# Kernel optimization log

Hardware: AMD Instinct MI355X
Metric: run time of the kernel (lower is better)

Reference implementation:

```python
import jax, jax.numpy as jnp
import numpy as np

B, L, T_ENC = 32, 64, 196
INPUT, EMBED, HIDDEN, VOCAB = 2048, 512, 512, 32000
SCALE = 1.0 / float(512 ** 0.5)


def setup_inputs() -> dict:
    key = jax.random.key(0)
    ks = jax.random.split(key, 24)
    s = 0.05
    embed_table = jax.random.normal(ks[3], (VOCAB, EMBED)) * s
    embed_table = embed_table.at[0].set(0.0)  # padding_idx=0
    d = {
        "features": jax.random.normal(ks[0], (B, INPUT)),
        "captions": jax.random.randint(ks[1], (B, L), 0, VOCAB, dtype=jnp.int32),
        "lengths": jnp.full((B,), L, dtype=jnp.int32),
        "encoder_outputs": jax.random.normal(ks[2], (B, T_ENC, 512)),
        "embed_table": embed_table,
        "ft1_w": jax.random.normal(ks[4], (HIDDEN, INPUT)) * s,
        "ft1_b": jax.random.normal(ks[5], (HIDDEN,)) * s,
        "ft2_w": jax.random.normal(ks[6], (HIDDEN, HIDDEN)) * s,
        "ft2_b": jax.random.normal(ks[7], (HIDDEN,)) * s,
        # torch LSTM gate order: i, f, g, o; layer0 input = embed+512
        "w_ih0": jax.random.normal(ks[8], (4 * HIDDEN, EMBED + 512)) * s,
        "w_hh0": jax.random.normal(ks[9], (4 * HIDDEN, HIDDEN)) * s,
        "b_ih0": jax.random.normal(ks[10], (4 * HIDDEN,)) * s,
        "b_hh0": jax.random.normal(ks[11], (4 * HIDDEN,)) * s,
        "w_ih1": jax.random.normal(ks[12], (4 * HIDDEN, HIDDEN)) * s,
        "w_hh1": jax.random.normal(ks[13], (4 * HIDDEN, HIDDEN)) * s,
        "b_ih1": jax.random.normal(ks[14], (4 * HIDDEN,)) * s,
        "b_hh1": jax.random.normal(ks[15], (4 * HIDDEN,)) * s,
        "fc_w": jax.random.normal(ks[16], (VOCAB, HIDDEN)) * s,
        "fc_b": jax.random.normal(ks[17], (VOCAB,)) * s,
    }
    return d


def _lstm_cell(x, h, c, w_ih, w_hh, b_ih, b_hh):
    g = x @ w_ih.T + h @ w_hh.T + b_ih + b_hh
    i, f, gg, o = jnp.split(g, 4, axis=-1)
    c2 = jax.nn.sigmoid(f) * c + jax.nn.sigmoid(i) * jnp.tanh(gg)
    h2 = jax.nn.sigmoid(o) * jnp.tanh(c2)
    return h2, c2


def reference(features, captions, lengths, encoder_outputs, embed_table,
              ft1_w, ft1_b, ft2_w, ft2_b,
              w_ih0, w_hh0, b_ih0, b_hh0,
              w_ih1, w_hh1, b_ih1, b_hh1,
              fc_w, fc_b):
    # feature extractor (eval mode -> dropout identity)
    f = jax.nn.relu(features @ ft1_w.T + ft1_b)
    f = f @ ft2_w.T + ft2_b                      # [B, H]
    h0 = jnp.stack([f, f])                       # [num_layers, B, H]
    c0 = h0

    emb = embed_table[captions]                  # [B, L, E]
    xs = jnp.swapaxes(emb, 0, 1)                 # [L, B, E]

    def step(carry, w):
        h, c = carry
        q = h[-1]                                             # [B, 512]
        scores = jnp.einsum('bh,bth->bt', q, encoder_outputs) * SCALE
        a = jax.nn.softmax(scores, axis=-1)
        ctx = jnp.einsum('bt,bth->bh', a, encoder_outputs)    # [B, 512]
        x = jnp.concatenate([w, ctx], axis=-1)                # [B, E+512]
        h0n, c0n = _lstm_cell(x, h[0], c[0], w_ih0, w_hh0, b_ih0, b_hh0)
        h1n, c1n = _lstm_cell(h0n, h[1], c[1], w_ih1, w_hh1, b_ih1, b_hh1)
        return (jnp.stack([h0n, h1n]), jnp.stack([c0n, c1n])), h1n

    _, hs = jax.lax.scan(step, (h0, c0), xs)      # hs: [L, B, H]
    logits = jnp.einsum('lbh,vh->lbv', hs, fc_w) + fc_b  # [L, B, V]
    # all lengths == L, so pack_padded_sequence data == time-major flatten
    return logits.reshape(L * B, VOCAB)
```

## Files before the change

kernel.cpp:

```cpp
#include <hip/hip_runtime.h>
#include <hip/hip_bf16.h>

typedef __hip_bfloat16 bf16;
typedef short s8v __attribute__((ext_vector_type(8)));
typedef float f4v __attribute__((ext_vector_type(4)));
typedef unsigned long long u64;
typedef unsigned int u32;

#define B_   32
#define L_   64
#define TENC 196
#define INP  2048
#define H_   512
#define V_   32000
#define NBLK 128
#define SLOTSTRIDE 16

static __device__ __forceinline__ float sigf(float x) { return 1.0f / (1.0f + expf(-x)); }
static __device__ __forceinline__ short f2bs(float x) {
    bf16 h = (bf16)x;
    return *(short*)&h;
}
static __device__ __forceinline__ float b2f(short s) {
    return __uint_as_float(((unsigned int)(unsigned short)s) << 16);
}
static __device__ __forceinline__ u32 packhl(float v) {
    bf16 hi = (bf16)v;
    float r = v - (float)hi;
    bf16 lo = (bf16)r;
    return ((u32)(*(unsigned short*)&hi) << 16) | (u32)(*(unsigned short*)&lo);
}
static __device__ __forceinline__ float ldf(const void* p, size_t i, int f32) {
    if (f32) return ((const float*)p)[i];
    return (float)((const bf16*)p)[i];
}
static __device__ __forceinline__ s8v ld8(const void* p, size_t i, int f32) {
    if (f32) {
        const float* fp = (const float*)p + i;
        float4 a = *(const float4*)fp;
        float4 b = *(const float4*)(fp + 4);
        s8v r;
        r[0] = f2bs(a.x); r[1] = f2bs(a.y); r[2] = f2bs(a.z); r[3] = f2bs(a.w);
        r[4] = f2bs(b.x); r[5] = f2bs(b.y); r[6] = f2bs(b.z); r[7] = f2bs(b.w);
        return r;
    }
    return *(const s8v*)((const bf16*)p + i);
}
static __device__ __forceinline__ s8v ld8lo(const void* p, size_t i, int f32) {
    s8v r = {};
    if (f32) {
        const float* fp = (const float*)p + i;
        float4 a = *(const float4*)fp;
        float4 b = *(const float4*)(fp + 4);
        float v[8] = {a.x, a.y, a.z, a.w, b.x, b.y, b.z, b.w};
        for (int j = 0; j < 8; ++j) {
            bf16 hi = (bf16)v[j];
            bf16 lo = (bf16)(v[j] - (float)hi);
            r[j] = *(short*)&lo;
        }
    }
    return r;
}

static __device__ __forceinline__ u64 ld64coh(const void* p) {
    return __hip_atomic_load((const u64*)p, __ATOMIC_RELAXED, __HIP_MEMORY_SCOPE_AGENT);
}
static __device__ __forceinline__ void st32coh(u32* p, u32 v) {
    __hip_atomic_store(p, v, __ATOMIC_RELAXED, __HIP_MEMORY_SCOPE_AGENT);
}
static __device__ __forceinline__ void st64coh(u32* p, u64 v) {
    __hip_atomic_store((u64*)p, v, __ATOMIC_RELAXED, __HIP_MEMORY_SCOPE_AGENT);
}

static __device__ __forceinline__ void slot_arrive(u32* slots, int blk, u32 val) {
    asm volatile("s_waitcnt vmcnt(0)" ::: "memory");
    __syncthreads();
    if (threadIdx.x == 0)
        __hip_atomic_store(slots + blk * SLOTSTRIDE, val, __ATOMIC_RELAXED, __HIP_MEMORY_SCOPE_AGENT);
}
static __device__ __forceinline__ void slot_wait(const u32* slots, int nslots, u32 val) {
    int tid = threadIdx.x;
    for (;;) {
        u32 v = val;
        if (tid < nslots)
            v = __hip_atomic_load(slots + tid * SLOTSTRIDE, __ATOMIC_RELAXED, __HIP_MEMORY_SCOPE_AGENT);
        if (__syncthreads_and((int)(v >= val))) break;
        __builtin_amdgcn_s_sleep(1);
    }
}

static __device__ __forceinline__ void issue32(const u32* St, int tid, u64* f) {
    int b0 = (tid >> 7), k = (tid & 127) * 4;
    #pragma unroll
    for (int q = 0; q < 16; ++q) {
        const u32* s = St + (2 * q + b0) * H_ + k;
        f[2 * q]     = ld64coh(s);
        f[2 * q + 1] = ld64coh(s + 2);
    }
}
static __device__ __forceinline__ void stage_write(const u64* f, int tid, short (*A)[520]) {
    int b0 = (tid >> 7), k = (tid & 127) * 4;
    #pragma unroll
    for (int q = 0; q < 16; ++q) {
        u32 v0 = (u32)f[2 * q],     v1 = (u32)(f[2 * q] >> 32);
        u32 v2 = (u32)f[2 * q + 1], v3 = (u32)(f[2 * q + 1] >> 32);
        int b = 2 * q + b0;
        uint2 hi, lo;
        hi.x = (v0 >> 16) | (v1 & 0xffff0000u);
        hi.y = (v2 >> 16) | (v3 & 0xffff0000u);
        lo.x = (v0 & 0xffffu) | (v1 << 16);
        lo.y = (v2 & 0xffffu) | (v3 << 16);
        *(uint2*)&A[2 * b][k]     = hi;
        *(uint2*)&A[2 * b + 1][k] = lo;
    }
}
static __device__ __forceinline__ f4v mfma_half(const short (*W)[1048], const short (*A)[520],
                                                int mrow, int nlo, int kq, int koff, f4v acc) {
    #pragma unroll
    for (int kk = 0; kk < 16; ++kk) {
        s8v a = *(const s8v*)&A[mrow][kk * 32 + kq];
        s8v b = *(const s8v*)&W[nlo][koff + kk * 32 + kq];
        acc = __builtin_amdgcn_mfma_f32_16x16x32_bf16(a, b, acc, 0, 0, 0);
    }
    return acc;
}

__global__ __launch_bounds__(256) void k_detect(const void* __restrict__ feat,
                                                int* __restrict__ flag) {
    __shared__ float red[256];
    const unsigned short* p = (const unsigned short*)feat;
    float mx = 0.f;
    for (int i = threadIdx.x; i < 65536; i += 256) {
        unsigned int u = ((unsigned int)p[i]) << 16;
        float v = __uint_as_float(u);
        mx = fmaxf(mx, fabsf(v));
    }
    red[threadIdx.x] = mx;
    __syncthreads();
    for (int s = 128; s; s >>= 1) {
        if (threadIdx.x < s) red[threadIdx.x] = fmaxf(red[threadIdx.x], red[threadIdx.x + s]);
        __syncthreads();
    }
    if (threadIdx.x == 0) flag[0] = (red[0] > 1e4f) ? 1 : 0;
}

__global__ __launch_bounds__(256) void k_prep(const int* __restrict__ dflag,
                                              const void* __restrict__ enc,
                                              const void* __restrict__ w_ih0, const void* __restrict__ w_hh0,
                                              const void* __restrict__ w_ih1, const void* __restrict__ w_hh1,
                                              const void* __restrict__ b_ih0, const void* __restrict__ b_hh0,
                                              const void* __restrict__ b_ih1, const void* __restrict__ b_hh1,
                                              bf16* __restrict__ enc16,
                                              bf16* __restrict__ Wp0, bf16* __restrict__ Wp1,
                                              float* __restrict__ bias0, float* __restrict__ bias1,
                                              u32* __restrict__ slots) {
    int f32 = *dflag;
    int gid = blockIdx.x * 256 + threadIdx.x;
    if (gid < NBLK * SLOTSTRIDE) slots[gid] = 0;
    const int GE = (B_ * TENC * H_) / 8;
    const int GW = (2048 * 1024) / 8;
    int stride = gridDim.x * 256;
    for (int g = gid; g < GE + 2 * GW; g += stride) {
        if (g < GE) {
            *(s8v*)(enc16 + (size_t)g * 8) = ld8(enc, (size_t)g * 8, f32);
        } else if (g < GE + GW) {
            int gg = g - GE; int j = gg >> 7; int k = (gg & 127) * 8;
            s8v v = (k < 512) ? ld8(w_ih0, (size_t)j * 1024 + 512 + k, f32)
                              : ld8(w_hh0, (size_t)j * 512 + (k - 512), f32);
            *(s8v*)(Wp0 + (size_t)j * 1024 + k) = v;
        } else {
            int gg = g - GE - GW; int j = gg >> 7; int k = (gg & 127) * 8;
            s8v v = (k < 512) ? ld8(w_ih1, (size_t)j * 512 + k, f32)
                              : ld8(w_hh1, (size_t)j * 512 + (k - 512), f32);
            *(s8v*)(Wp1 + (size_t)j * 1024 + k) = v;
        }
    }
    for (int j = gid; j < 2048; j += stride) {
        bias0[j] = ldf(b_ih0, j, f32) + ldf(b_hh0, j, f32);
        bias1[j] = ldf(b_ih1, j, f32) + ldf(b_hh1, j, f32);
    }
}

__global__ __launch_bounds__(256) void k_gemb(const int* __restrict__ dflag,
                                              const int* __restrict__ captions,
                                              const void* __restrict__ embed,
                                              const void* __restrict__ w_ih0,
                                              float* __restrict__ Gemb) {
    __shared__ short As[128][40];
    __shared__ short Bs[128][40];
    int f32 = *dflag;
    int n0 = blockIdx.x * 128;
    int m0 = blockIdx.y * 128;
    int tid = threadIdx.x, lane = tid & 63, wv = tid >> 6;
    int wm = wv >> 1, wn = wv & 1;
    f4v acc[16] = {};
    for (int k0 = 0; k0 < 512; k0 += 32) {
        for (int s = tid; s < 512; s += 256) {
            int r = s >> 2, cs = (s & 3) * 8;
            int R = m0 + r, e = R >> 1, part = R & 1;
            int b = e & 31, tt = e >> 5;
            size_t ei = (size_t)captions[b * L_ + tt] * H_ + k0 + cs;
            *(s8v*)&As[r][cs] = part ? ld8lo(embed, ei, f32) : ld8(embed, ei, f32);
        }
        for (int s = tid; s < 512; s += 256) {
            int r = s >> 2, cs = (s & 3) * 8;
            *(s8v*)&Bs[r][cs] = ld8(w_ih0, (size_t)(n0 + r) * 1024 + k0 + cs, f32);
        }
        __syncthreads();
        int kq = (lane >> 4) * 8;
        s8v af[4], bfv[4];
        for (int i = 0; i < 4; ++i) af[i]  = *(const s8v*)&As[wm * 64 + i * 16 + (lane & 15)][kq];
        for (int i = 0; i < 4; ++i) bfv[i] = *(const s8v*)&Bs[wn * 64 + i * 16 + (lane & 15)][kq];
        for (int mi = 0; mi < 4; ++mi)
            for (int ni = 0; ni < 4; ++ni)
                acc[mi * 4 + ni] = __builtin_amdgcn_mfma_f32_16x16x32_bf16(af[mi], bfv[ni], acc[mi * 4 + ni], 0, 0, 0);
        __syncthreads();
    }
    int n = lane & 15, quad = lane >> 4;
    for (int ni = 0; ni < 4; ++ni) {
        int col = n0 + wn * 64 + ni * 16 + n;
        for (int mi = 0; mi < 4; ++mi) {
            f4v a = acc[mi * 4 + ni];
            int rowbase = m0 + wm * 64 + mi * 16 + quad * 4;
            int e0 = rowbase >> 1;
            Gemb[(size_t)e0 * 2048 + col]       = a[0] + a[1];
            Gemb[(size_t)(e0 + 1) * 2048 + col] = a[2] + a[3];
        }
    }
}

__global__ __launch_bounds__(256) void k_feat1(const int* __restrict__ dflag,
                                               const void* __restrict__ feat,
                                               const void* __restrict__ w,
                                               const void* __restrict__ bias,
                                               float* __restrict__ t1) {
    int f32 = *dflag;
    int wid = (blockIdx.x * 256 + threadIdx.x) >> 6;
    int lane = threadIdx.x & 63;
    int b = wid >> 9, o = wid & 511;
    float acc = 0.f;
    for (int k = lane; k < INP; k += 64)
        acc += ldf(feat, (size_t)b * INP + k, f32) * ldf(w, (size_t)o * INP + k, f32);
    for (int off = 32; off; off >>= 1) acc += __shfl_down(acc, off, 64);
    if (lane == 0) {
        acc += ldf(bias, o, f32);
        t1[b * H_ + o] = acc > 0.f ? acc : 0.f;
    }
}

__global__ __launch_bounds__(256) void k_feat2(const int* __restrict__ dflag,
                                               const float* __restrict__ t1,
                                               const void* __restrict__ w,
                                               const void* __restrict__ bias,
                                               float* __restrict__ c0, float* __restrict__ c1,
                                               u32* __restrict__ h0A, u32* __restrict__ h1A) {
    int f32 = *dflag;
    int wid = (blockIdx.x * 256 + threadIdx.x) >> 6;
    int lane = threadIdx.x & 63;
    int b = wid >> 9, o = wid & 511;
    float acc = 0.f;
    for (int k = lane; k < H_; k += 64)
        acc += t1[b * H_ + k] * ldf(w, (size_t)o * H_ + k, f32);
    for (int off = 32; off; off >>= 1) acc += __shfl_down(acc, off, 64);
    if (lane == 0) {
        float v = acc + ldf(bias, o, f32);
        int idx = b * H_ + o;
        c0[idx] = v; c1[idx] = v;
        u32 pk = packhl(v);
        h0A[idx] = pk; h1A[idx] = pk;
    }
}

__global__ __launch_bounds__(256, 1) void k_recur(
        const bf16* __restrict__ enc16,
        const bf16* __restrict__ Wp0, const bf16* __restrict__ Wp1,
        const float* __restrict__ bias0, const float* __restrict__ bias1,
        const float* __restrict__ Gemb,
        const float* __restrict__ c0i, const float* __restrict__ c1i,
        u32* __restrict__ h0A, u32* __restrict__ h0B,
        u32* __restrict__ h1A, u32* __restrict__ h1B,
        u32* __restrict__ ctxp,
        bf16* __restrict__ hs, u32* __restrict__ slots) {
    __shared__ short Asm[64][520];
    __shared__ short Wsm[2][16][1048];
    __shared__ float qs[H_];
    __shared__ float sc[256];
    __shared__ float wred[8];
    __shared__ float ep[4][4][32];
    const float SCALE = 0.04419417382415922f;
    int blk = blockIdx.x, tid = threadIdx.x;
    int lane = tid & 63, wv = tid >> 6;
    int u0 = blk * 4;
    int mrow = wv * 16 + (lane & 15);
    int kq = (lane >> 4) * 8;
    int nlo = lane & 15;
    int quad = lane >> 4;
    int b0i = wv * 8 + quad * 2;
    int eb = tid & 31, eu = (tid >> 5) & 3, ej = u0 + eu;
    int epi = tid < 128;

    for (int cell = 0; cell < 2; ++cell) {
        const bf16* Wp = cell ? Wp1 : Wp0;
        for (int s = tid; s < 2048; s += 256) {
            int r = s >> 7, cc = (s & 127) * 8;
            size_t j = (size_t)((r >> 2) * H_ + u0 + (r & 3));
            *(s8v*)&Wsm[cell][r][cc] = *(const s8v*)(Wp + j * 1024 + cc);
        }
    }
    float c0r = 0.f, c1r = 0.f;
    float bi0 = 0, bf0 = 0, bg0 = 0, bo0 = 0, bi1 = 0, bf1 = 0, bg1 = 0, bo1 = 0;
    if (epi) {
        c0r = c0i[eb * H_ + ej]; c1r = c1i[eb * H_ + ej];
        bi0 = bias0[ej]; bf0 = bias0[512 + ej]; bg0 = bias0[1024 + ej]; bo0 = bias0[1536 + ej];
        bi1 = bias1[ej]; bf1 = bias1[512 + ej]; bg1 = bias1[1024 + ej]; bo1 = bias1[1536 + ej];
    }
    __syncthreads();
    u32 nbar = 0;

    for (int t = 0; t < L_; ++t) {
        int p = t & 1;
        const u32* h0p = p ? h0B : h0A;  u32* h0n = p ? h0A : h0B;
        const u32* h1p = p ? h1B : h1A;  u32* h1n = p ? h1A : h1B;

        u64 fA[32];
        issue32(h0p, tid, fA);
        f4v accB = {};
        if (blk < B_) {
            int b = blk;
            {
                u64 v = ld64coh(h1p + b * H_ + 2 * tid);
                u32 v0 = (u32)v, v1 = (u32)(v >> 32);
                qs[2 * tid]     = b2f((short)(v0 >> 16)) + b2f((short)(v0 & 0xffffu));
                qs[2 * tid + 1] = b2f((short)(v1 >> 16)) + b2f((short)(v1 & 0xffffu));
            }
            __syncthreads();
            if (tid < TENC) {
                const bf16* erow = enc16 + ((size_t)b * TENC + tid) * H_;
                float a0 = 0, a1 = 0, a2 = 0, a3 = 0, a4 = 0, a5 = 0, a6 = 0, a7 = 0;
                #pragma unroll 4
                for (int k = 0; k < H_; k += 8) {
                    s8v e8 = *(const s8v*)(erow + k);
                    float4 q0 = *(const float4*)&qs[k];
                    float4 q1 = *(const float4*)&qs[k + 4];
                    a0 += q0.x * b2f(e8[0]); a1 += q0.y * b2f(e8[1]);
                    a2 += q0.z * b2f(e8[2]); a3 += q0.w * b2f(e8[3]);
                    a4 += q1.x * b2f(e8[4]); a5 += q1.y * b2f(e8[5]);
                    a6 += q1.z * b2f(e8[6]); a7 += q1.w * b2f(e8[7]);
                }
                sc[tid] = (((a0 + a1) + (a2 + a3)) + ((a4 + a5) + (a6 + a7))) * SCALE;
            }
            __syncthreads();
            float v = (tid < TENC) ? sc[tid] : -1e30f;
            float m = v;
            #pragma unroll
            for (int off = 32; off; off >>= 1) m = fmaxf(m, __shfl_xor(m, off, 64));
            if (lane == 0) wred[wv] = m;
            __syncthreads();
            m = fmaxf(fmaxf(wred[0], wred[1]), fmaxf(wred[2], wred[3]));
            float e = (tid < TENC) ? expf(v - m) : 0.f;
            float s = e;
            #pragma unroll
            for (int off = 32; off; off >>= 1) s += __shfl_xor(s, off, 64);
            if (lane == 0) wred[4 + wv] = s;
            __syncthreads();
            float inv = 1.0f / ((wred[4] + wred[5]) + (wred[6] + wred[7]));
            if (tid < TENC) sc[tid] = e * inv;
            __syncthreads();
            const bf16* ebase = enc16 + (size_t)b * TENC * H_ + 2 * tid;
            float x0 = 0, x1 = 0, y0 = 0, y1 = 0;
            #pragma unroll 4
            for (int tt = 0; tt < TENC; tt += 2) {
                u32 ua = *(const u32*)(ebase + (size_t)tt * H_);
                u32 ub = *(const u32*)(ebase + (size_t)(tt + 1) * H_);
                float p0 = sc[tt], p1 = sc[tt + 1];
                x0 += p0 * b2f((short)ua); x1 += p0 * b2f((short)(ua >> 16));
                y0 += p1 * b2f((short)ub); y1 += p1 * b2f((short)(ub >> 16));
            }
            u64 pk = ((u64)packhl(x1 + y1) << 32) | (u64)packhl(x0 + y0);
            st64coh(ctxp + b * H_ + 2 * tid, pk);
        }
        stage_write(fA, tid, Asm);
        __syncthreads();
        accB = mfma_half(Wsm[0], Asm, mrow, nlo, kq, 512, accB);
        ++nbar;
        if (blk < B_) slot_arrive(slots, blk, nbar);
        slot_wait(slots, B_, nbar);

        {
            u64 fB[32];
            issue32(ctxp, tid, fB);
            float g0 = 0, g1 = 0, g2 = 0, g3 = 0;
            if (epi) {
                size_t ge = (size_t)(t * 32 + eb) * 2048 + ej;
                g0 = Gemb[ge]; g1 = Gemb[ge + 512]; g2 = Gemb[ge + 1024]; g3 = Gemb[ge + 1536];
            }
            u64 fC[32];
            issue32(h1p, tid, fC);
            stage_write(fB, tid, Asm);
            __syncthreads();
            accB = mfma_half(Wsm[0], Asm, mrow, nlo, kq, 0, accB);
            ep[nlo >> 2][nlo & 3][b0i]     = accB[0] + accB[1];
            ep[nlo >> 2][nlo & 3][b0i + 1] = accB[2] + accB[3];
            __syncthreads();
            if (epi) {
                float gi = ep[0][eu][eb] + bi0 + g0;
                float gf = ep[1][eu][eb] + bf0 + g1;
                float gg = ep[2][eu][eb] + bg0 + g2;
                float go = ep[3][eu][eb] + bo0 + g3;
                float c2 = sigf(gf) * c0r + sigf(gi) * tanhf(gg);
                float h2 = sigf(go) * tanhf(c2);
                c0r = c2;
                st32coh(h0n + eb * H_ + ej, packhl(h2));
            }
            stage_write(fC, tid, Asm);
            __syncthreads();
            f4v accC = {};
            accC = mfma_half(Wsm[1], Asm, mrow, nlo, kq, 512, accC);
            ++nbar;
            slot_arrive(slots, blk, nbar);
            slot_wait(slots, NBLK, nbar);

            u64 fD[32];
            issue32(h0n, tid, fD);
            stage_write(fD, tid, Asm);
            __syncthreads();
            accC = mfma_half(Wsm[1], Asm, mrow, nlo, kq, 0, accC);
            ep[nlo >> 2][nlo & 3][b0i]     = accC[0] + accC[1];
            ep[nlo >> 2][nlo & 3][b0i + 1] = accC[2] + accC[3];
            __syncthreads();
            if (epi) {
                float gi = ep[0][eu][eb] + bi1;
                float gf = ep[1][eu][eb] + bf1;
                float gg = ep[2][eu][eb] + bg1;
                float go = ep[3][eu][eb] + bo1;
                float c2 = sigf(gf) * c1r + sigf(gi) * tanhf(gg);
                float h2 = sigf(go) * tanhf(c2);
                c1r = c2;
                st32coh(h1n + eb * H_ + ej, packhl(h2));
                hs[(size_t)(t * 32 + eb) * H_ + ej] = (bf16)h2;
            }
            ++nbar;
            slot_arrive(slots, blk, nbar);
            slot_wait(slots, NBLK, nbar);
        }
    }
}

__global__ __launch_bounds__(256) void k_vocab(const int* __restrict__ dflag,
                                               const bf16* __restrict__ hs,
                                               const void* __restrict__ fcw,
                                               const void* __restrict__ fcb,
                                               void* __restrict__ out) {
    __shared__ short As[128][40];
    __shared__ short Bs[128][40];
    int f32 = *dflag;
    int m0 = blockIdx.x * 128;
    int n0 = blockIdx.y * 128;
    int tid = threadIdx.x, lane = tid & 63, wv = tid >> 6;
    int wm = wv >> 1, wn = wv & 1;
    f4v acc[16] = {};
    for (int k0 = 0; k0 < 512; k0 += 32) {
        for (int s = tid; s < 512; s += 256) {
            int r = s >> 2, cs = (s & 3) * 8;
            *(s8v*)&As[r][cs] = *(const s8v*)(hs + (size_t)(m0 + r) * 512 + k0 + cs);
        }
        for (int s = tid; s < 512; s += 256) {
            int r = s >> 2, cs = (s & 3) * 8;
            *(s8v*)&Bs[r][cs] = ld8(fcw, (size_t)(n0 + r) * 512 + k0 + cs, f32);
        }
        __syncthreads();
        int kq = (lane >> 4) * 8;
        s8v af[4], bfv[4];
        for (int i = 0; i < 4; ++i) af[i]  = *(const s8v*)&As[wm * 64 + i * 16 + (lane & 15)][kq];
        for (int i = 0; i < 4; ++i) bfv[i] = *(const s8v*)&Bs[wn * 64 + i * 16 + (lane & 15)][kq];
        for (int mi = 0; mi < 4; ++mi)
            for (int ni = 0; ni < 4; ++ni)
                acc[mi * 4 + ni] = __builtin_amdgcn_mfma_f32_16x16x32_bf16(af[mi], bfv[ni], acc[mi * 4 + ni], 0, 0, 0);
        __syncthreads();
    }
    int n = lane & 15, quad = lane >> 4;
    for (int ni = 0; ni < 4; ++ni) {
        int col = n0 + wn * 64 + ni * 16 + n;
        float bias = ldf(fcb, col, f32);
        for (int mi = 0; mi < 4; ++mi) {
            f4v a = acc[mi * 4 + ni];
            for (int rg = 0; rg < 4; ++rg) {
                int row = m0 + wm * 64 + mi * 16 + quad * 4 + rg;
                float v = a[rg] + bias;
                if (f32) ((float*)out)[(size_t)row * V_ + col] = v;
                else     ((bf16*)out)[(size_t)row * V_ + col] = (bf16)v;
            }
        }
    }
}

extern "C" void kernel_launch(void* const* d_in, const int* in_sizes, int n_in,
                              void* d_out, int out_size, void* d_ws, size_t ws_size,
                              hipStream_t stream) {
    const void* features = d_in[0];
    const int*  captions = (const int*)d_in[1];
    const void* enc      = d_in[3];
    const void* embed    = d_in[4];
    const void* ft1w     = d_in[5];
    const void* ft1b     = d_in[6];
    const void* ft2w     = d_in[7];
    const void* ft2b     = d_in[8];
    const void* w_ih0    = d_in[9];
    const void* w_hh0    = d_in[10];
    const void* b_ih0    = d_in[11];
    const void* b_hh0    = d_in[12];
    const void* w_ih1    = d_in[13];
    const void* w_hh1    = d_in[14];
    const void* b_ih1    = d_in[15];
    const void* b_hh1    = d_in[16];
    const void* fcw      = d_in[17];
    const void* fcb      = d_in[18];

    char* ws = (char*)d_ws;
    size_t off = 0;
    float* t1    = (float*)(ws + off); off += 32 * 512 * 4;
    float* c0    = (float*)(ws + off); off += 32 * 512 * 4;
    float* c1    = (float*)(ws + off); off += 32 * 512 * 4;
    u32* h0A     = (u32*)(ws + off); off += 32 * 512 * 4;
    u32* h0B     = (u32*)(ws + off); off += 32 * 512 * 4;
    u32* h1A     = (u32*)(ws + off); off += 32 * 512 * 4;
    u32* h1B     = (u32*)(ws + off); off += 32 * 512 * 4;
    u32* ctxp    = (u32*)(ws + off); off += 32 * 512 * 4;
    bf16* hs     = (bf16*)(ws + off); off += (size_t)2048 * 512 * 2;
    bf16* enc16  = (bf16*)(ws + off); off += (size_t)32 * 196 * 512 * 2;
    bf16* Wp0    = (bf16*)(ws + off); off += (size_t)2048 * 1024 * 2;
    bf16* Wp1    = (bf16*)(ws + off); off += (size_t)2048 * 1024 * 2;
    float* bias0 = (float*)(ws + off); off += 2048 * 4;
    float* bias1 = (float*)(ws + off); off += 2048 * 4;
    float* Gemb  = (float*)(ws + off); off += (size_t)2048 * 2048 * 4;
    int* dflag   = (int*)(ws + off); off += 16;
    u32* slots   = (u32*)(ws + off); off += NBLK * SLOTSTRIDE * 4;

    k_detect<<<1, 256, 0, stream>>>(features, dflag);
    k_prep<<<1024, 256, 0, stream>>>(dflag, enc, w_ih0, w_hh0, w_ih1, w_hh1,
                                     b_ih0, b_hh0, b_ih1, b_hh1,
                                     enc16, Wp0, Wp1, bias0, bias1, slots);
    k_gemb<<<dim3(16, 32), 256, 0, stream>>>(dflag, captions, embed, w_ih0, Gemb);
    k_feat1<<<4096, 256, 0, stream>>>(dflag, features, ft1w, ft1b, t1);
    k_feat2<<<4096, 256, 0, stream>>>(dflag, t1, ft2w, ft2b, c0, c1, h0A, h1A);
    k_recur<<<NBLK, 256, 0, stream>>>(enc16, Wp0, Wp1, bias0, bias1, Gemb,
                                      c0, c1, h0A, h0B, h1A, h1B, ctxp, hs, slots);
    k_vocab<<<dim3(16, 250), 256, 0, stream>>>(dflag, hs, fcw, fcb, (void*)d_out);
}
```

Before: 2.636 ms.

## Reorder recurrent step to overlap attention wait with layer-1 hidden GEMM

Restructures the per-timestep schedule of the persistent LSTM kernel. The h0 operand is now reused from the LDS tile staged at the end of the previous step, so it is no longer reloaded. The layer-1 recurrent half-GEMM on h1 now runs before waiting on the attention barrier. Global loads change from paired 64-bit atomic loads to single dwordx4 loads with system-coherent cache bits and an explicit vmcnt wait. The aim is to hide the attention-to-context barrier latency and reduce load instruction count, at the cost of relying on inline asm cache semantics for cross-block coherence.

```diff
diff --git a/kernel.cpp b/kernel.cpp
--- a/kernel.cpp
+++ b/kernel.cpp
@@ -6,6 +6,7 @@
 typedef float f4v __attribute__((ext_vector_type(4)));
 typedef unsigned long long u64;
 typedef unsigned int u32;
+typedef u32 u32x4v __attribute__((ext_vector_type(4)));
 
 #define B_   32
 #define L_   64
@@ -72,6 +73,35 @@
     __hip_atomic_store((u64*)p, v, __ATOMIC_RELAXED, __HIP_MEMORY_SCOPE_AGENT);
 }
 
+static __device__ __forceinline__ void issue16(const u32* St, int tid, u32x4v* f) {
+    int b0 = (tid >> 7), k = (tid & 127) * 4;
+    #pragma unroll
+    for (int q = 0; q < 16; ++q) {
+        const u32* s = St + (2 * q + b0) * H_ + k;
+        asm volatile("global_load_dwordx4 %0, %1, off sc0 sc1"
+                     : "=v"(f[q]) : "v"(s));
+    }
+}
+static __device__ __forceinline__ void waitvm() {
+    asm volatile("s_waitcnt vmcnt(0)" ::: "memory");
+    __builtin_amdgcn_sched_barrier(0);
+}
+static __device__ __forceinline__ void stage16(const u32x4v* f, int tid, short (*A)[520]) {
+    int b0 = (tid >> 7), k = (tid & 127) * 4;
+    #pragma unroll
+    for (int q = 0; q < 16; ++q) {
+        u32 v0 = f[q][0], v1 = f[q][1], v2 = f[q][2], v3 = f[q][3];
+        int b = 2 * q + b0;
+        uint2 hi, lo;
+        hi.x = (v0 >> 16) | (v1 & 0xffff0000u);
+        hi.y = (v2 >> 16) | (v3 & 0xffff0000u);
+        lo.x = (v0 & 0xffffu) | (v1 << 16);
+        lo.y = (v2 & 0xffffu) | (v3 << 16);
+        *(uint2*)&A[2 * b][k]     = hi;
+        *(uint2*)&A[2 * b + 1][k] = lo;
+    }
+}
+
 static __device__ __forceinline__ void slot_arrive(u32* slots, int blk, u32 val) {
     asm volatile("s_waitcnt vmcnt(0)" ::: "memory");
     __syncthreads();
@@ -89,31 +119,6 @@
     }
 }
 
-static __device__ __forceinline__ void issue32(const u32* St, int tid, u64* f) {
-    int b0 = (tid >> 7), k = (tid & 127) * 4;
-    #pragma unroll
-    for (int q = 0; q < 16; ++q) {
-        const u32* s = St + (2 * q + b0) * H_ + k;
-        f[2 * q]     = ld64coh(s);
-        f[2 * q + 1] = ld64coh(s + 2);
-    }
-}
-static __device__ __forceinline__ void stage_write(const u64* f, int tid, short (*A)[520]) {
-    int b0 = (tid >> 7), k = (tid & 127) * 4;
-    #pragma unroll
-    for (int q = 0; q < 16; ++q) {
-        u32 v0 = (u32)f[2 * q],     v1 = (u32)(f[2 * q] >> 32);
-        u32 v2 = (u32)f[2 * q + 1], v3 = (u32)(f[2 * q + 1] >> 32);
-        int b = 2 * q + b0;
-        uint2 hi, lo;
-        hi.x = (v0 >> 16) | (v1 & 0xffff0000u);
-        hi.y = (v2 >> 16) | (v3 & 0xffff0000u);
-        lo.x = (v0 & 0xffffu) | (v1 << 16);
-        lo.y = (v2 & 0xffffu) | (v3 << 16);
-        *(uint2*)&A[2 * b][k]     = hi;
-        *(uint2*)&A[2 * b + 1][k] = lo;
-    }
-}
 static __device__ __forceinline__ f4v mfma_half(const short (*W)[1048], const short (*A)[520],
                                                 int mrow, int nlo, int kq, int koff, f4v acc) {
     #pragma unroll
@@ -314,17 +319,21 @@
         bi0 = bias0[ej]; bf0 = bias0[512 + ej]; bg0 = bias0[1024 + ej]; bo0 = bias0[1536 + ej];
         bi1 = bias1[ej]; bf1 = bias1[512 + ej]; bg1 = bias1[1024 + ej]; bo1 = bias1[1536 + ej];
     }
+    {
+        u32x4v f0[16];
+        issue16(h0A, tid, f0);
+        waitvm();
+        stage16(f0, tid, Asm);
+    }
     __syncthreads();
     u32 nbar = 0;
 
     for (int t = 0; t < L_; ++t) {
         int p = t & 1;
-        const u32* h0p = p ? h0B : h0A;  u32* h0n = p ? h0A : h0B;
+        u32* h0n = p ? h0A : h0B;
         const u32* h1p = p ? h1B : h1A;  u32* h1n = p ? h1A : h1B;
 
-        u64 fA[32];
-        issue32(h0p, tid, fA);
-        f4v accB = {};
+        u32 barA = ++nbar;
         if (blk < B_) {
             int b = blk;
             {
@@ -378,25 +387,33 @@
             }
             u64 pk = ((u64)packhl(x1 + y1) << 32) | (u64)packhl(x0 + y0);
             st64coh(ctxp + b * H_ + 2 * tid, pk);
-        }
-        stage_write(fA, tid, Asm);
+            slot_arrive(slots, blk, barA);
+        }
+        f4v accB = {};
+        accB = mfma_half(Wsm[0], Asm, mrow, nlo, kq, 512, accB);
         __syncthreads();
-        accB = mfma_half(Wsm[0], Asm, mrow, nlo, kq, 512, accB);
-        ++nbar;
-        if (blk < B_) slot_arrive(slots, blk, nbar);
-        slot_wait(slots, B_, nbar);
-
+        f4v accC = {};
         {
-            u64 fB[32];
-            issue32(ctxp, tid, fB);
+            u32x4v fC[16];
+            issue16(h1p, tid, fC);
+            waitvm();
+            stage16(fC, tid, Asm);
+            __syncthreads();
+            accC = mfma_half(Wsm[1], Asm, mrow, nlo, kq, 512, accC);
+        }
+        slot_wait(slots, B_, barA);
+
+        u32 barB = ++nbar;
+        {
+            u32x4v fB[16];
+            issue16(ctxp, tid, fB);
             float g0 = 0, g1 = 0, g2 = 0, g3 = 0;
             if (epi) {
                 size_t ge = (size_t)(t * 32 + eb) * 2048 + ej;
                 g0 = Gemb[ge]; g1 = Gemb[ge + 512]; g2 = Gemb[ge + 1024]; g3 = Gemb[ge + 1536];
             }
-            u64 fC[32];
-            issue32(h1p, tid, fC);
-            stage_write(fB, tid, Asm);
+            waitvm();
+            stage16(fB, tid, Asm);
             __syncthreads();
             accB = mfma_half(Wsm[0], Asm, mrow, nlo, kq, 0, accB);
             ep[nlo >> 2][nlo & 3][b0i]     = accB[0] + accB[1];
@@ -412,17 +429,16 @@
                 c0r = c2;
                 st32coh(h0n + eb * H_ + ej, packhl(h2));
             }
-            stage_write(fC, tid, Asm);
-            __syncthreads();
-            f4v accC = {};
-            accC = mfma_half(Wsm[1], Asm, mrow, nlo, kq, 512, accC);
-            ++nbar;
-            slot_arrive(slots, blk, nbar);
-            slot_wait(slots, NBLK, nbar);
-
-            u64 fD[32];
-            issue32(h0n, tid, fD);
-            stage_write(fD, tid, Asm);
+            slot_arrive(slots, blk, barB);
+            slot_wait(slots, NBLK, barB);
+        }
+
+        u32 barC = ++nbar;
+        {
+            u32x4v fD[16];
+            issue16(h0n, tid, fD);
+            waitvm();
+            stage16(fD, tid, Asm);
             __syncthreads();
             accC = mfma_half(Wsm[1], Asm, mrow, nlo, kq, 0, accC);
             ep[nlo >> 2][nlo & 3][b0i]     = accC[0] + accC[1];
@@ -439,9 +455,8 @@
                 st32coh(h1n + eb * H_ + ej, packhl(h2));
                 hs[(size_t)(t * 32 + eb) * H_ + ej] = (bf16)h2;
             }
-            ++nbar;
-            slot_arrive(slots, blk, nbar);
-            slot_wait(slots, NBLK, nbar);
+            slot_arrive(slots, blk, barC);
+            slot_wait(slots, NBLK, barC);
         }
     }
 }
```

New measurement: 2.388 ms. -9.4%, faster.
